# Kernel tuning notes

Hardware: AMD Instinct MI355X
Metric: run time of the kernel (lower is better)

Reference implementation:

```python
import jax, jax.numpy as jnp
import numpy as np

D_Q = D_K = D_V = 1024
H = 16
D_ATT = 64
NQ = NK = 4096
EPS = 1e-12


def setup_inputs() -> dict:
    key = jax.random.key(0)
    ks = jax.random.split(key, 12)
    s_in = 1.0 / np.sqrt(D_Q)
    s_out = 1.0 / np.sqrt(H * D_ATT)
    return {
        "queries": jax.random.normal(ks[0], (NQ, D_Q), jnp.float32),
        "keys": jax.random.normal(ks[1], (NK, D_K), jnp.float32),
        "values": jax.random.normal(ks[2], (NK, D_V), jnp.float32),
        "Wq": jax.random.uniform(ks[3], (D_Q, H * D_ATT), jnp.float32, -s_in, s_in),
        "bq": jax.random.uniform(ks[4], (H * D_ATT,), jnp.float32, -s_in, s_in),
        "Wk": jax.random.uniform(ks[5], (D_K, H * D_ATT), jnp.float32, -s_in, s_in),
        "bk": jax.random.uniform(ks[6], (H * D_ATT,), jnp.float32, -s_in, s_in),
        "Wv": jax.random.uniform(ks[7], (D_V, H * D_ATT), jnp.float32, -s_in, s_in),
        "bv": jax.random.uniform(ks[8], (H * D_ATT,), jnp.float32, -s_in, s_in),
        "Wo": jax.random.uniform(ks[9], (H * D_ATT, D_Q), jnp.float32, -s_out, s_out),
        "bo": jax.random.uniform(ks[10], (D_Q,), jnp.float32, -s_out, s_out),
        "gamma": jnp.ones((D_Q,), jnp.float32),
        "beta": jnp.zeros((D_Q,), jnp.float32),
    }


def reference(queries, keys, values, Wq, bq, Wk, bk, Wv, bv, Wo, bo, gamma, beta):
    nq = queries.shape[0]
    nk = keys.shape[0]
    # projections -> (n, h, d)
    q = (queries @ Wq + bq).reshape(nq, H, D_ATT)
    k = (keys @ Wk + bk).reshape(nk, H, D_ATT)
    v = (values @ Wv + bv).reshape(nk, H, D_ATT)
    # scores (h, nq, nk)
    att = jnp.einsum("qhd,khd->hqk", q, k) / np.sqrt(D_ATT).astype(np.float32)
    att = jax.nn.softmax(att, axis=-1)  # dropout = identity (eval)
    out = jnp.einsum("hqk,khd->qhd", att, v).reshape(nq, H * D_ATT)
    out = queries + out @ Wo + bo
    # LayerNorm, eps=1e-12
    mu = jnp.mean(out, axis=-1, keepdims=True)
    var = jnp.mean(jnp.square(out - mu), axis=-1, keepdims=True)
    out = (out - mu) * jax.lax.rsqrt(var + EPS) * gamma + beta
    return out
```

## Files before the change

### kernel.cpp

```cpp
#include <hip/hip_runtime.h>
#include <stdint.h>

typedef unsigned short u16;
typedef unsigned int u32;
typedef __attribute__((ext_vector_type(8))) __bf16 bf16x8;
typedef __attribute__((ext_vector_type(2))) __bf16 bf16x2;
typedef __attribute__((ext_vector_type(4))) float f32x4;
typedef __attribute__((ext_vector_type(16))) float f32x16;
typedef __attribute__((ext_vector_type(8))) u16 u16x8;
typedef __attribute__((ext_vector_type(4))) u32 u32x4;

#define Q_SCALE 0.1803368801111204f

__device__ __forceinline__ float ex2(float x) { return __builtin_amdgcn_exp2f(x); }

__device__ __forceinline__ u16 f2bf(float f) {
  __bf16 h = (__bf16)f;
  return __builtin_bit_cast(u16, h);
}
__device__ __forceinline__ float bf2f(u16 u) {
  u32 x = ((u32)u) << 16;
  return __builtin_bit_cast(float, x);
}
__device__ __forceinline__ u32 pack2(float a, float b) {
  bf16x2 v; v.x = (__bf16)a; v.y = (__bf16)b;
  return __builtin_bit_cast(u32, v);
}
__device__ __forceinline__ void gl_lds16(const void* g, void* l) {
  __builtin_amdgcn_global_load_lds((const __attribute__((address_space(1))) void*)g,
                                   (__attribute__((address_space(3))) void*)l, 16, 0, 0);
}

__global__ __launch_bounds__(256) void prep_kernel(const float* __restrict__ q,
                                                   const float* __restrict__ k,
                                                   const float* __restrict__ v,
                                                   u16* __restrict__ xdst,
                                                   const float* __restrict__ Wq,
                                                   const float* __restrict__ Wk,
                                                   const float* __restrict__ Wv,
                                                   const float* __restrict__ Wo,
                                                   u16* __restrict__ wcatT,
                                                   u16* __restrict__ woT) {
  __shared__ u16 tile[64][72];
  int z = blockIdx.z;
  int t = threadIdx.x;
  if (z == 4) {
    int b = blockIdx.y * 16 + blockIdx.x;
#pragma unroll 4
    for (int it = 0; it < 24; ++it) {
      size_t tt = (size_t)b * 6144 + it * 256 + t;
      size_t e = tt * 8;
      int which = (int)(e >> 22);
      const float* s = which == 0 ? q : which == 1 ? k : v;
      size_t off = e & 4194303;
      float4 a = *(const float4*)(s + off);
      float4 bb = *(const float4*)(s + off + 4);
      u16x8 o;
      o[0] = f2bf(a.x); o[1] = f2bf(a.y); o[2] = f2bf(a.z); o[3] = f2bf(a.w);
      o[4] = f2bf(bb.x); o[5] = f2bf(bb.y); o[6] = f2bf(bb.z); o[7] = f2bf(bb.w);
      *(u16x8*)(xdst + e) = o;
    }
    return;
  }
  const float* W = z == 0 ? Wq : z == 1 ? Wk : z == 2 ? Wv : Wo;
  int k0 = blockIdx.y * 64, n0 = blockIdx.x * 64;
  int r = t >> 2, c0 = (t & 3) * 16;
  const float* src = W + (size_t)(k0 + r) * 1024 + n0 + c0;
#pragma unroll
  for (int i = 0; i < 16; i += 4) {
    float4 x = *(const float4*)(src + i);
    tile[r][c0 + i] = f2bf(x.x); tile[r][c0 + i + 1] = f2bf(x.y);
    tile[r][c0 + i + 2] = f2bf(x.z); tile[r][c0 + i + 3] = f2bf(x.w);
  }
  __syncthreads();
  int n = t >> 2, kc = (t & 3) * 16;
  u16x8 o0, o1;
#pragma unroll
  for (int j = 0; j < 8; ++j) { o0[j] = tile[kc + j][n]; o1[j] = tile[kc + 8 + j][n]; }
  u16* dst = (z < 3) ? (wcatT + (size_t)z * 1048576 + (size_t)(n0 + n) * 1024 + k0 + kc)
                     : (woT + (size_t)(n0 + n) * 1024 + k0 + kc);
  *(u16x8*)dst = o0;
  *(u16x8*)(dst + 8) = o1;
}

__global__ __launch_bounds__(256) void gemm_bt(const u16* __restrict__ A,
                                               const u16* __restrict__ BT,
                                               u16* __restrict__ outBF,
                                               const float* __restrict__ b0,
                                               const float* __restrict__ b1,
                                               const float* __restrict__ b2) {
  __shared__ u16 As[2][4096];
  __shared__ u16 Bs[2][4096];
  int tid = threadIdx.x;
  int bid = blockIdx.y * 8 + blockIdx.x;
  int cpx = gridDim.y;
  int swz = (bid & 7) * cpx + (bid >> 3);
  int m0 = (swz >> 3) * 128, n0 = (swz & 7) * 128;
  const u16* bt = BT + (size_t)(m0 >> 12) * 1048576;
  int w = tid >> 6, l = tid & 63;
  int wr = w >> 1, wc = w & 1;
  f32x4 acc[4][4];
#pragma unroll
  for (int i = 0; i < 4; ++i)
#pragma unroll
    for (int j = 0; j < 4; ++j)
#pragma unroll
      for (int rr = 0; rr < 4; ++rr) acc[i][j][rr] = 0.f;

  auto stage = [&](int buf, int kt) {
#pragma unroll
    for (int i = 0; i < 2; ++i) {
      int id = i * 256 + tid;
      int r = id >> 2, cp = id & 3;
      int cl = cp ^ ((r ^ (r >> 2)) & 3);
      gl_lds16(A + (size_t)(m0 + r) * 1024 + kt * 32 + cl * 8, &As[buf][id * 8]);
      gl_lds16(bt + (size_t)(n0 + r) * 1024 + kt * 32 + cl * 8, &Bs[buf][id * 8]);
    }
  };
  stage(0, 0);
  __syncthreads();
  int sw = (l & 3) ^ ((l >> 2) & 3);
  int phys = (l >> 4) ^ sw;
  for (int kt = 0; kt < 32; ++kt) {
    int buf = kt & 1;
    if (kt < 31) stage(buf ^ 1, kt + 1);
    bf16x8 af[4], bfr[4];
#pragma unroll
    for (int mi = 0; mi < 4; ++mi) {
      int row = wr * 64 + mi * 16 + (l & 15);
      af[mi] = *(const bf16x8*)&As[buf][row * 32 + phys * 8];
    }
#pragma unroll
    for (int nj = 0; nj < 4; ++nj) {
      int rowb = wc * 64 + nj * 16 + (l & 15);
      bfr[nj] = *(const bf16x8*)&Bs[buf][rowb * 32 + phys * 8];
    }
#pragma unroll
    for (int mi = 0; mi < 4; ++mi)
#pragma unroll
      for (int nj = 0; nj < 4; ++nj)
        acc[mi][nj] = __builtin_amdgcn_mfma_f32_16x16x32_bf16(af[mi], bfr[nj],
                                                              acc[mi][nj], 0, 0, 0);
    __syncthreads();
  }
#pragma unroll
  for (int mi = 0; mi < 4; ++mi)
#pragma unroll
    for (int nj = 0; nj < 4; ++nj)
#pragma unroll
      for (int rr = 0; rr < 4; ++rr) {
        int row = m0 + wr * 64 + mi * 16 + (l >> 4) * 4 + rr;
        int col = n0 + wc * 64 + nj * 16 + (l & 15);
        float vv = acc[mi][nj][rr];
        int sec = row >> 12, orow = row & 4095;
        const float* bp = sec == 0 ? b0 : sec == 1 ? b1 : b2;
        vv += bp[col];
        if (sec == 0) vv *= Q_SCALE;
        outBF[(size_t)sec * 4194304 + (size_t)orow * 1024 + col] = f2bf(vv);
      }
}

__global__ __launch_bounds__(256) void gemm_n64(const u16* __restrict__ A,
                                                const u16* __restrict__ BT,
                                                float* __restrict__ outF,
                                                const float* __restrict__ b0,
                                                const float* __restrict__ resid) {
  __shared__ u16 As[2][4096];
  __shared__ u16 Bs[2][2048];
  int tid = threadIdx.x;
  int bid = blockIdx.y * 8 + blockIdx.x;
  int swz = (bid & 7) * 64 + (bid >> 3);
  int m0 = (swz >> 4) * 128, n0 = (swz & 15) * 64;
  int w = tid >> 6, l = tid & 63;
  int wr = w >> 1, wc = w & 1;
  f32x4 acc[4][2];
#pragma unroll
  for (int i = 0; i < 4; ++i)
#pragma unroll
    for (int j = 0; j < 2; ++j)
#pragma unroll
      for (int rr = 0; rr < 4; ++rr) acc[i][j][rr] = 0.f;

  auto stage = [&](int buf, int kt) {
#pragma unroll
    for (int i = 0; i < 2; ++i) {
      int id = i * 256 + tid;
      int r = id >> 2, cp = id & 3;
      int cl = cp ^ ((r ^ (r >> 2)) & 3);
      gl_lds16(A + (size_t)(m0 + r) * 1024 + kt * 32 + cl * 8, &As[buf][id * 8]);
    }
    {
      int id = tid;
      int r = id >> 2, cp = id & 3;
      int cl = cp ^ ((r ^ (r >> 2)) & 3);
      gl_lds16(BT + (size_t)(n0 + r) * 1024 + kt * 32 + cl * 8, &Bs[buf][id * 8]);
    }
  };
  stage(0, 0);
  __syncthreads();
  int sw = (l & 3) ^ ((l >> 2) & 3);
  int phys = (l >> 4) ^ sw;
  for (int kt = 0; kt < 32; ++kt) {
    int buf = kt & 1;
    if (kt < 31) stage(buf ^ 1, kt + 1);
    bf16x8 af[4], bfr[2];
#pragma unroll
    for (int mi = 0; mi < 4; ++mi) {
      int row = wr * 64 + mi * 16 + (l & 15);
      af[mi] = *(const bf16x8*)&As[buf][row * 32 + phys * 8];
    }
#pragma unroll
    for (int nj = 0; nj < 2; ++nj) {
      int rowb = wc * 32 + nj * 16 + (l & 15);
      bfr[nj] = *(const bf16x8*)&Bs[buf][rowb * 32 + phys * 8];
    }
#pragma unroll
    for (int mi = 0; mi < 4; ++mi)
#pragma unroll
      for (int nj = 0; nj < 2; ++nj)
        acc[mi][nj] = __builtin_amdgcn_mfma_f32_16x16x32_bf16(af[mi], bfr[nj],
                                                              acc[mi][nj], 0, 0, 0);
    __syncthreads();
  }
#pragma unroll
  for (int mi = 0; mi < 4; ++mi)
#pragma unroll
    for (int nj = 0; nj < 2; ++nj)
#pragma unroll
      for (int rr = 0; rr < 4; ++rr) {
        int row = m0 + wr * 64 + mi * 16 + (l >> 4) * 4 + rr;
        int col = n0 + wc * 32 + nj * 16 + (l & 15);
        outF[(size_t)row * 1024 + col] =
            acc[mi][nj][rr] + b0[col] + resid[(size_t)row * 1024 + col];
      }
}

__global__ __launch_bounds__(256) void vtrans_kernel(const u16* __restrict__ vp,
                                                     u16* __restrict__ vt) {
  __shared__ u16 tile[64][72];
  int t = threadIdx.x;
  int n0 = blockIdx.x * 64, h = blockIdx.y;
  int r = t >> 2, c0 = (t & 3) * 16;
  u16x8 a = *(const u16x8*)(vp + (size_t)(n0 + r) * 1024 + h * 64 + c0);
  u16x8 b = *(const u16x8*)(vp + (size_t)(n0 + r) * 1024 + h * 64 + c0 + 8);
#pragma unroll
  for (int j = 0; j < 8; ++j) { tile[r][c0 + j] = a[j]; tile[r][c0 + 8 + j] = b[j]; }
  __syncthreads();
  int d = t >> 2, nc = (t & 3) * 16;
  u16x8 o0, o1;
#pragma unroll
  for (int j = 0; j < 8; ++j) { o0[j] = tile[nc + j][d]; o1[j] = tile[nc + 8 + j][d]; }
  size_t base = (size_t)(h * 64 + d) * 4096 + n0 + nc;
  *(u16x8*)(vt + base) = o0;
  *(u16x8*)(vt + base + 8) = o1;
}

__global__ __launch_bounds__(512, 4) void attn_kernel(const u16* __restrict__ qp,
                                                      const u16* __restrict__ kp,
                                                      const u16* __restrict__ vt,
                                                      u16* __restrict__ attout) {
  __shared__ u16 smem[32768];
  int tid = threadIdx.x;
  int w = tid >> 6, l = tid & 63;
  int half = w >> 2, wl = w & 3;
  int hi = l >> 5, l31 = l & 31, l7 = l & 7;
  int h = blockIdx.y, bx = blockIdx.x;
  int qrow = bx * 128 + wl * 32 + l31;
  bf16x8 qf[4];
#pragma unroll
  for (int ds = 0; ds < 4; ++ds)
    qf[ds] = *(const bf16x8*)(qp + (size_t)qrow * 1024 + h * 64 + ds * 16 + hi * 8);

  f32x16 zero16;
#pragma unroll
  for (int r = 0; r < 16; ++r) zero16[r] = 0.f;
  f32x16 accO[2];
#pragma unroll
  for (int r = 0; r < 16; ++r) { accO[0][r] = 0.f; accO[1][r] = 0.f; }
  float l_run = 0.f;

  u16* sbase = smem + half * 16384;
  int ht = (wl << 6) | l;
  const u16* srcK[2]; const u16* srcV[2]; int dstOff[2];
#pragma unroll
  for (int i = 0; i < 2; ++i) {
    int id = i * 256 + ht;
    int r = id >> 3, cp = id & 7;
    int cl = cp ^ ((r ^ (r >> 3)) & 7);
    srcK[i] = kp + (size_t)(half * 2048 + r) * 1024 + h * 64 + cl * 8;
    srcV[i] = vt + (size_t)(h * 64 + r) * 4096 + half * 2048 + cl * 8;
    dstOff[i] = id * 8;
  }
  auto stage = [&](int buf, int kt) {
    u16* b = sbase + buf * 8192;
#pragma unroll
    for (int i = 0; i < 2; ++i) {
      gl_lds16(srcK[i] + (size_t)kt * 65536, b + dstOff[i]);
      gl_lds16(srcV[i] + kt * 64, b + 4096 + dstOff[i]);
    }
  };
  stage(0, 0);
  __syncthreads();

  for (int kt = 0; kt < 32; ++kt) {
    int buf = kt & 1;
    if (kt < 31) stage(buf ^ 1, kt + 1);
    const u16* Kt = sbase + buf * 8192;
    const u16* Vt = Kt + 4096;

    f32x16 accS[2];
    __builtin_amdgcn_s_setprio(1);
#pragma unroll
    for (int mt = 0; mt < 2; ++mt) {
      int row = mt * 32 + l31;
      int g = (row ^ (row >> 3)) & 7;
      {
        bf16x8 kf = *(const bf16x8*)(Kt + row * 64 + ((0 + hi) ^ g) * 8);
        accS[mt] = __builtin_amdgcn_mfma_f32_32x32x16_bf16(kf, qf[0], zero16, 0, 0, 0);
      }
#pragma unroll
      for (int ds = 1; ds < 4; ++ds) {
        int phys = (2 * ds + hi) ^ g;
        bf16x8 kf = *(const bf16x8*)(Kt + row * 64 + phys * 8);
        accS[mt] = __builtin_amdgcn_mfma_f32_32x32x16_bf16(kf, qf[ds], accS[mt], 0, 0, 0);
      }
    }
    __builtin_amdgcn_s_setprio(0);

    u32 pku[2][8];
    float s0 = 0.f, s1 = 0.f, s2 = 0.f, s3 = 0.f;
#pragma unroll
    for (int mt = 0; mt < 2; ++mt)
#pragma unroll
      for (int qd = 0; qd < 8; ++qd) {
        float a = ex2(accS[mt][2 * qd]);
        float b = ex2(accS[mt][2 * qd + 1]);
        if (qd & 1) { s2 += a; s3 += b; } else { s0 += a; s1 += b; }
        pku[mt][qd] = pack2(a, b);
      }
    float t1 = (s0 + s1) + (s2 + s3);
    t1 += __shfl_xor(t1, 32, 64);
    l_run += t1;

    bf16x8 pb[4];
#pragma unroll
    for (int ks = 0; ks < 4; ++ks) {
      const int mt = ks >> 1, k1 = ks & 1;
      u32 a0 = pku[mt][4 * k1 + 0], c0 = pku[mt][4 * k1 + 2];
      u32 a1 = pku[mt][4 * k1 + 1], c1 = pku[mt][4 * k1 + 3];
      asm("v_permlane32_swap_b32 %0, %1" : "+v"(a0), "+v"(c0));
      asm("v_permlane32_swap_b32 %0, %1" : "+v"(a1), "+v"(c1));
      u32x4 fr;
      fr[0] = a0; fr[1] = a1; fr[2] = c0; fr[3] = c1;
      pb[ks] = __builtin_bit_cast(bf16x8, fr);
    }
    __builtin_amdgcn_s_setprio(1);
#pragma unroll
    for (int mto = 0; mto < 2; ++mto) {
      int row = mto * 32 + l31;
      int g = (row ^ (row >> 3)) & 7;
#pragma unroll
      for (int ks = 0; ks < 4; ++ks) {
        int phys = (2 * ks + hi) ^ g;
        bf16x8 vf = *(const bf16x8*)(Vt + row * 64 + phys * 8);
        accO[mto] = __builtin_amdgcn_mfma_f32_32x32x16_bf16(vf, pb[ks], accO[mto], 0, 0, 0);
      }
    }
    __builtin_amdgcn_s_setprio(0);
    __syncthreads();
  }

  u16* pO = smem;
  float* ml = (float*)(smem + 2 * 128 * 72);
  int q = wl * 32 + l31;
#pragma unroll
  for (int mto = 0; mto < 2; ++mto)
#pragma unroll
    for (int g = 0; g < 4; ++g)
#pragma unroll
      for (int j = 0; j < 2; ++j) {
        int r = g * 4 + j * 2;
        int d = j * 2 + 8 * g + 4 * hi + 32 * mto;
        u32 pk = pack2(accO[mto][r], accO[mto][r + 1]);
        *(u32*)&pO[(size_t)(half * 128 + q) * 72 + d] = pk;
      }
  if (hi == 0) ml[half * 128 + q] = l_run;
  __syncthreads();
  {
    int qq = tid >> 2, d0 = (tid & 3) * 16;
    float invL = 1.f / (ml[qq] + ml[128 + qq]);
    u16x8 ra0 = *(u16x8*)&pO[(size_t)qq * 72 + d0];
    u16x8 ra1 = *(u16x8*)&pO[(size_t)qq * 72 + d0 + 8];
    u16x8 rb0 = *(u16x8*)&pO[(size_t)(128 + qq) * 72 + d0];
    u16x8 rb1 = *(u16x8*)&pO[(size_t)(128 + qq) * 72 + d0 + 8];
    u16x8 o0, o1;
#pragma unroll
    for (int j = 0; j < 8; ++j) {
      o0[j] = f2bf((bf2f(ra0[j]) + bf2f(rb0[j])) * invL);
      o1[j] = f2bf((bf2f(ra1[j]) + bf2f(rb1[j])) * invL);
    }
    size_t ob = (size_t)(bx * 128 + qq) * 1024 + (size_t)h * 64 + d0;
    *(u16x8*)(attout + ob) = o0;
    *(u16x8*)(attout + ob + 8) = o1;
  }
}

__global__ __launch_bounds__(256) void ln_kernel(float* __restrict__ io,
                                                 const float* __restrict__ gamma,
                                                 const float* __restrict__ beta) {
  int row = blockIdx.x, t = threadIdx.x;
  float4 v = *(const float4*)(io + (size_t)row * 1024 + t * 4);
  float s = v.x + v.y + v.z + v.w;
  float sq = v.x * v.x + v.y * v.y + v.z * v.z + v.w * v.w;
#pragma unroll
  for (int off = 1; off < 64; off <<= 1) {
    s += __shfl_xor(s, off, 64);
    sq += __shfl_xor(sq, off, 64);
  }
  __shared__ float rs[4], rq[4];
  if ((t & 63) == 0) { rs[t >> 6] = s; rq[t >> 6] = sq; }
  __syncthreads();
  float S = rs[0] + rs[1] + rs[2] + rs[3];
  float Q = rq[0] + rq[1] + rq[2] + rq[3];
  float mu = S * (1.f / 1024.f);
  float var = Q * (1.f / 1024.f) - mu * mu;
  float invs = rsqrtf(var + 1e-12f);
  float4 g = *(const float4*)(gamma + t * 4);
  float4 b = *(const float4*)(beta + t * 4);
  float4 o;
  o.x = (v.x - mu) * invs * g.x + b.x;
  o.y = (v.y - mu) * invs * g.y + b.y;
  o.z = (v.z - mu) * invs * g.z + b.z;
  o.w = (v.w - mu) * invs * g.w + b.w;
  *(float4*)(io + (size_t)row * 1024 + t * 4) = o;
}

extern "C" void kernel_launch(void* const* d_in, const int* in_sizes, int n_in,
                              void* d_out, int out_size, void* d_ws, size_t ws_size,
                              hipStream_t stream) {
  (void)in_sizes; (void)n_in; (void)out_size; (void)ws_size;
  const float* queries = (const float*)d_in[0];
  const float* keys    = (const float*)d_in[1];
  const float* values  = (const float*)d_in[2];
  const float* Wq = (const float*)d_in[3];
  const float* bq = (const float*)d_in[4];
  const float* Wk = (const float*)d_in[5];
  const float* bk = (const float*)d_in[6];
  const float* Wv = (const float*)d_in[7];
  const float* bv = (const float*)d_in[8];
  const float* Wo = (const float*)d_in[9];
  const float* bo = (const float*)d_in[10];
  const float* gamma = (const float*)d_in[11];
  const float* beta  = (const float*)d_in[12];
  float* out = (float*)d_out;

  u16* ws = (u16*)d_ws;
  u16* xq     = ws;
  u16* attout = ws;
  u16* vt     = ws + 4194304;
  u16* wcatT  = ws + 12582912;
  u16* woT    = ws + 15728640;
  u16* qp     = ws + 16777216;
  u16* kp     = qp + 4194304;
  u16* vp     = qp + 8388608;

  prep_kernel<<<dim3(16, 16, 5), dim3(256), 0, stream>>>(queries, keys, values, xq,
                                                         Wq, Wk, Wv, Wo, wcatT, woT);
  gemm_bt<<<dim3(8, 96), dim3(256), 0, stream>>>(xq, wcatT, qp, bq, bk, bv);
  vtrans_kernel<<<dim3(64, 16), dim3(256), 0, stream>>>(vp, vt);
  attn_kernel<<<dim3(32, 16), dim3(512), 0, stream>>>(qp, kp, vt, attout);
  gemm_n64<<<dim3(8, 64), dim3(256), 0, stream>>>(attout, woT, out, bo, queries);
  ln_kernel<<<dim3(4096), dim3(256), 0, stream>>>(out, gamma, beta);
}
```

Baseline: 174.5 us.

## Halve attention K/V tile to 32 keys to cut LDS and raise occupancy

```diff
diff --git a/kernel.cpp b/kernel.cpp
--- a/kernel.cpp
+++ b/kernel.cpp
@@ -255,15 +255,15 @@
   *(u16x8*)(vt + base + 8) = o1;
 }
 
-__global__ __launch_bounds__(512, 4) void attn_kernel(const u16* __restrict__ qp,
+__global__ __launch_bounds__(512, 8) void attn_kernel(const u16* __restrict__ qp,
                                                       const u16* __restrict__ kp,
                                                       const u16* __restrict__ vt,
                                                       u16* __restrict__ attout) {
-  __shared__ u16 smem[32768];
+  __shared__ u16 smem[19456];
   int tid = threadIdx.x;
   int w = tid >> 6, l = tid & 63;
   int half = w >> 2, wl = w & 3;
-  int hi = l >> 5, l31 = l & 31, l7 = l & 7;
+  int hi = l >> 5, l31 = l & 31;
   int h = blockIdx.y, bx = blockIdx.x;
   int qrow = bx * 128 + wl * 32 + l31;
   bf16x8 qf[4];
@@ -271,107 +271,92 @@
   for (int ds = 0; ds < 4; ++ds)
     qf[ds] = *(const bf16x8*)(qp + (size_t)qrow * 1024 + h * 64 + ds * 16 + hi * 8);
 
-  f32x16 zero16;
-#pragma unroll
-  for (int r = 0; r < 16; ++r) zero16[r] = 0.f;
   f32x16 accO[2];
 #pragma unroll
   for (int r = 0; r < 16; ++r) { accO[0][r] = 0.f; accO[1][r] = 0.f; }
   float l_run = 0.f;
 
-  u16* sbase = smem + half * 16384;
+  u16* sbase = smem + half * 8192;
   int ht = (wl << 6) | l;
-  const u16* srcK[2]; const u16* srcV[2]; int dstOff[2];
-#pragma unroll
-  for (int i = 0; i < 2; ++i) {
-    int id = i * 256 + ht;
-    int r = id >> 3, cp = id & 7;
-    int cl = cp ^ ((r ^ (r >> 3)) & 7);
-    srcK[i] = kp + (size_t)(half * 2048 + r) * 1024 + h * 64 + cl * 8;
-    srcV[i] = vt + (size_t)(h * 64 + r) * 4096 + half * 2048 + cl * 8;
-    dstOff[i] = id * 8;
-  }
+  int rK = ht >> 3, cpK = ht & 7;
+  int clK = cpK ^ ((rK ^ (rK >> 3)) & 7);
+  const u16* srcK = kp + (size_t)(half * 2048 + rK) * 1024 + h * 64 + clK * 8;
+  int dV = ht >> 2, cpV = ht & 3;
+  int clV = cpV ^ (((dV >> 1) ^ (dV >> 3)) & 3);
+  const u16* srcV = vt + (size_t)(h * 64 + dV) * 4096 + half * 2048 + clV * 8;
+  int dstK = ht * 8, dstV = 2048 + ht * 8;
   auto stage = [&](int buf, int kt) {
-    u16* b = sbase + buf * 8192;
-#pragma unroll
-    for (int i = 0; i < 2; ++i) {
-      gl_lds16(srcK[i] + (size_t)kt * 65536, b + dstOff[i]);
-      gl_lds16(srcV[i] + kt * 64, b + 4096 + dstOff[i]);
-    }
+    u16* b = sbase + buf * 4096;
+    gl_lds16(srcK + (size_t)kt * 32768, b + dstK);
+    gl_lds16(srcV + kt * 32, b + dstV);
   };
   stage(0, 0);
   __syncthreads();
 
-  for (int kt = 0; kt < 32; ++kt) {
+  int gK = (l31 ^ (l31 >> 3)) & 7;
+  int gV = ((l31 >> 1) ^ (l31 >> 3)) & 3;
+
+  for (int kt = 0; kt < 64; ++kt) {
     int buf = kt & 1;
-    if (kt < 31) stage(buf ^ 1, kt + 1);
-    const u16* Kt = sbase + buf * 8192;
-    const u16* Vt = Kt + 4096;
-
-    f32x16 accS[2];
+    if (kt < 63) stage(buf ^ 1, kt + 1);
+    const u16* Kt = sbase + buf * 4096;
+    const u16* Vt = Kt + 2048;
+
+    f32x16 accS;
+#pragma unroll
+    for (int r = 0; r < 16; ++r) accS[r] = 0.f;
     __builtin_amdgcn_s_setprio(1);
 #pragma unroll
-    for (int mt = 0; mt < 2; ++mt) {
-      int row = mt * 32 + l31;
-      int g = (row ^ (row >> 3)) & 7;
-      {
-        bf16x8 kf = *(const bf16x8*)(Kt + row * 64 + ((0 + hi) ^ g) * 8);
-        accS[mt] = __builtin_amdgcn_mfma_f32_32x32x16_bf16(kf, qf[0], zero16, 0, 0, 0);
-      }
-#pragma unroll
-      for (int ds = 1; ds < 4; ++ds) {
-        int phys = (2 * ds + hi) ^ g;
-        bf16x8 kf = *(const bf16x8*)(Kt + row * 64 + phys * 8);
-        accS[mt] = __builtin_amdgcn_mfma_f32_32x32x16_bf16(kf, qf[ds], accS[mt], 0, 0, 0);
-      }
+    for (int ds = 0; ds < 4; ++ds) {
+      bf16x8 kf = *(const bf16x8*)(Kt + l31 * 64 + ((2 * ds + hi) ^ gK) * 8);
+      accS = __builtin_amdgcn_mfma_f32_32x32x16_bf16(kf, qf[ds], accS, 0, 0, 0);
     }
     __builtin_amdgcn_s_setprio(0);
 
-    u32 pku[2][8];
+    u32 pku[8];
     float s0 = 0.f, s1 = 0.f, s2 = 0.f, s3 = 0.f;
 #pragma unroll
-    for (int mt = 0; mt < 2; ++mt)
-#pragma unroll
-      for (int qd = 0; qd < 8; ++qd) {
-        float a = ex2(accS[mt][2 * qd]);
-        float b = ex2(accS[mt][2 * qd + 1]);
-        if (qd & 1) { s2 += a; s3 += b; } else { s0 += a; s1 += b; }
-        pku[mt][qd] = pack2(a, b);
-      }
+    for (int qd = 0; qd < 8; ++qd) {
+      float a = ex2(accS[2 * qd]);
+      float b = ex2(accS[2 * qd + 1]);
+      if (qd & 1) { s2 += a; s3 += b; } else { s0 += a; s1 += b; }
+      pku[qd] = pack2(a, b);
+    }
     float t1 = (s0 + s1) + (s2 + s3);
     t1 += __shfl_xor(t1, 32, 64);
     l_run += t1;
 
-    bf16x8 pb[4];
-#pragma unroll
-    for (int ks = 0; ks < 4; ++ks) {
-      const int mt = ks >> 1, k1 = ks & 1;
-      u32 a0 = pku[mt][4 * k1 + 0], c0 = pku[mt][4 * k1 + 2];
-      u32 a1 = pku[mt][4 * k1 + 1], c1 = pku[mt][4 * k1 + 3];
+    bf16x8 pb0, pb1;
+    {
+      u32 a0 = pku[0], c0 = pku[2], a1 = pku[1], c1 = pku[3];
       asm("v_permlane32_swap_b32 %0, %1" : "+v"(a0), "+v"(c0));
       asm("v_permlane32_swap_b32 %0, %1" : "+v"(a1), "+v"(c1));
-      u32x4 fr;
-      fr[0] = a0; fr[1] = a1; fr[2] = c0; fr[3] = c1;
-      pb[ks] = __builtin_bit_cast(bf16x8, fr);
+      u32x4 fr; fr[0] = a0; fr[1] = a1; fr[2] = c0; fr[3] = c1;
+      pb0 = __builtin_bit_cast(bf16x8, fr);
+      u32 a2 = pku[4], c2 = pku[6], a3 = pku[5], c3 = pku[7];
+      asm("v_permlane32_swap_b32 %0, %1" : "+v"(a2), "+v"(c2));
+      asm("v_permlane32_swap_b32 %0, %1" : "+v"(a3), "+v"(c3));
+      u32x4 fr2; fr2[0] = a2; fr2[1] = a3; fr2[2] = c2; fr2[3] = c3;
+      pb1 = __builtin_bit_cast(bf16x8, fr2);
     }
     __builtin_amdgcn_s_setprio(1);
-#pragma unroll
-    for (int mto = 0; mto < 2; ++mto) {
-      int row = mto * 32 + l31;
-      int g = (row ^ (row >> 3)) & 7;
-#pragma unroll
-      for (int ks = 0; ks < 4; ++ks) {
-        int phys = (2 * ks + hi) ^ g;
-        bf16x8 vf = *(const bf16x8*)(Vt + row * 64 + phys * 8);
-        accO[mto] = __builtin_amdgcn_mfma_f32_32x32x16_bf16(vf, pb[ks], accO[mto], 0, 0, 0);
-      }
+    {
+      bf16x8 vf;
+      vf = *(const bf16x8*)(Vt + l31 * 32 + ((0 + hi) ^ gV) * 8);
+      accO[0] = __builtin_amdgcn_mfma_f32_32x32x16_bf16(vf, pb0, accO[0], 0, 0, 0);
+      vf = *(const bf16x8*)(Vt + l31 * 32 + ((2 + hi) ^ gV) * 8);
+      accO[0] = __builtin_amdgcn_mfma_f32_32x32x16_bf16(vf, pb1, accO[0], 0, 0, 0);
+      vf = *(const bf16x8*)(Vt + (32 + l31) * 32 + ((0 + hi) ^ gV) * 8);
+      accO[1] = __builtin_amdgcn_mfma_f32_32x32x16_bf16(vf, pb0, accO[1], 0, 0, 0);
+      vf = *(const bf16x8*)(Vt + (32 + l31) * 32 + ((2 + hi) ^ gV) * 8);
+      accO[1] = __builtin_amdgcn_mfma_f32_32x32x16_bf16(vf, pb1, accO[1], 0, 0, 0);
     }
     __builtin_amdgcn_s_setprio(0);
     __syncthreads();
   }
 
   u16* pO = smem;
-  float* ml = (float*)(smem + 2 * 128 * 72);
+  float* ml = (float*)(smem + 18432);
   int q = wl * 32 + l31;
 #pragma unroll
   for (int mto = 0; mto < 2; ++mto)
```

Measured after the change: 361.8 us. +107.3%, slower.
